# Performance work log

Hardware: AMD Instinct MI355X
Metric: run time of the kernel (lower is better)

## Reference

```python
import jax, jax.numpy as jnp
import numpy as np

IN_DIM = 256
OUT_DIM = 256
GRID_SIZE = 8
K = 3  # spline_order
LOW, UP = -1.0, 1.0
BATCH = 512


def _control_grid():
    # equally spaced control points, extended by K on each side (paper sec 2.4)
    spacing = (UP - LOW) / GRID_SIZE
    g = jnp.arange(-K, GRID_SIZE + K + 1, dtype=jnp.float32) * spacing + LOW
    # buffer shape (out_dim, in_dim, G + 2K + 1)
    return jnp.broadcast_to(g[None, None, :], (OUT_DIM, IN_DIM, g.shape[0]))


def _bspline_bases(x, grid):
    # x: (B, in_dim); grid: (out, in, T). Cox-de Boor recursion.
    xx = x[:, None, :, None]          # (B, 1, in, 1)
    g = grid[None]                    # (1, out, in, T)
    # order-0 (piecewise-constant) bases
    b = ((xx >= g[..., :-1]) & (xx < g[..., 1:])).astype(x.dtype)
    for j in range(1, K + 1):
        b = (xx - g[..., :-(j + 1)]) / (g[..., j:-1] - g[..., :-(j + 1)]) * b[..., :-1] \
          + (g[..., j + 1:] - xx) / (g[..., j + 1:] - g[..., 1:-j]) * b[..., 1:]
    return b  # (B, out, in, G + K)


def setup_inputs() -> dict:
    key = jax.random.key(0)
    k1, k2, k3 = jax.random.split(key, 3)
    x = jax.random.normal(k1, (BATCH, IN_DIM), dtype=jnp.float32)
    # xavier_normal_ on (out, in, G+K): fan_in = in*(G+K) -> std = sqrt(2/(fan_in+fan_out))
    fan_out = IN_DIM * (GRID_SIZE + K)  # torch convention: dim0 = fan_out, rest = fan_in
    fan_in = OUT_DIM * (GRID_SIZE + K)
    std = float(np.sqrt(2.0 / (fan_in + fan_out)))
    coef = jax.random.normal(k2, (OUT_DIM, IN_DIM, GRID_SIZE + K), dtype=jnp.float32) * std
    residual_weight = jax.random.normal(k3, (OUT_DIM, IN_DIM), dtype=jnp.float32) * 0.1
    univariate_weight = jnp.ones((OUT_DIM, IN_DIM), dtype=jnp.float32)
    return {"x": x, "coef": coef, "residual_weight": residual_weight,
            "univariate_weight": univariate_weight}


def reference(x, coef, residual_weight, univariate_weight):
    grid = _control_grid()
    bases = _bspline_bases(x, grid)                      # (B, out, in, G+K)
    spline = jnp.einsum('boig,oig->boi', bases, coef)    # sum over grid dim
    phi = residual_weight[None, :, :] * jax.nn.silu(x)[:, None, :] \
        + univariate_weight[None, :, :] * spline          # (B, out, in)
    return jnp.sum(phi, axis=-1)                          # (B, out)
```

## Files before the change

kernel.cpp:

```cpp
#include <hip/hip_runtime.h>
#include <hip/hip_bf16.h>

typedef unsigned short ushort_t;
typedef unsigned int uint_t;
typedef __attribute__((ext_vector_type(8))) short short8;
typedef __attribute__((ext_vector_type(4))) float f32x4;

#define IN_DIM 256
#define OUT_DIM 256
#define NSPL 11
#define KSLOT 12
#define CHUNK_I 32
#define KC (CHUNK_I * KSLOT)
#define LSTRIDE (KC + 8)
#define NCHUNK 8
#define RAWF 356

__device__ __forceinline__ uint_t pk2(float lo, float hi) {
  __hip_bfloat162 h = __float22bfloat162_rn(make_float2(lo, hi));
  union { __hip_bfloat162 h2; uint_t u; } c; c.h2 = h;
  return c.u;
}

__device__ __forceinline__ void packA_scatter(ushort_t* cb, ushort_t* dump, float xf) {
  const float t = (xf + 1.75f) * 4.0f;
  const float fJ = floorf(t);
  const int J = (int)fJ;
  const float u = t - fJ;
  const float u2 = u * u, u3 = u2 * u, um = 1.0f - u;
  const float n0 = um * um * um * (1.0f / 6.0f);
  const float n1 = 0.5f * u3 - u2 + (4.0f / 6.0f);
  const float n2 = -0.5f * u3 + 0.5f * u2 + 0.5f * u + (1.0f / 6.0f);
  const float n3 = u3 * (1.0f / 6.0f);
  const float silu = xf / (1.0f + __expf(-xf));

#pragma unroll
  for (int s = 0; s < 12; ++s) cb[s] = 0;

  const uint_t p01 = pk2(n0, n1);
  const uint_t p23 = pk2(n2, n3);
  const uint_t psl = pk2(silu, silu);

  const int base = J - 3;
  ushort_t* w0 = ((unsigned)(base + 0) <= 10u) ? (cb + base + 0) : (dump + 0);
  ushort_t* w1 = ((unsigned)(base + 1) <= 10u) ? (cb + base + 1) : (dump + 1);
  ushort_t* w2 = ((unsigned)(base + 2) <= 10u) ? (cb + base + 2) : (dump + 2);
  ushort_t* w3 = ((unsigned)(base + 3) <= 10u) ? (cb + base + 3) : (dump + 3);
  *w0 = (ushort_t)p01;
  *w1 = (ushort_t)(p01 >> 16);
  *w2 = (ushort_t)p23;
  *w3 = (ushort_t)(p23 >> 16);
  cb[11] = (ushort_t)psl;
}

__device__ __forceinline__ void packW_f32(const float* c, float us, float r, uint_t o6[6]) {
  o6[0] = pk2(us * c[0], us * c[1]);
  o6[1] = pk2(us * c[2], us * c[3]);
  o6[2] = pk2(us * c[4], us * c[5]);
  o6[3] = pk2(us * c[6], us * c[7]);
  o6[4] = pk2(us * c[8], us * c[9]);
  o6[5] = pk2(us * c[10], r);
}

__device__ __forceinline__ void writeT(ushort_t* dst, const uint_t* p) {
  uint_t* d = (uint_t*)dst;
#pragma unroll
  for (int j = 0; j < 6; ++j) d[j] = p[j];
}

__global__ __launch_bounds__(256, 2) void fused(const float* __restrict__ x,
                                                const float* __restrict__ coef,
                                                const float* __restrict__ rw,
                                                const float* __restrict__ uw,
                                                float* __restrict__ out) {
  __shared__ __attribute__((aligned(16))) ushort_t As[2][16 * LSTRIDE];
  __shared__ __attribute__((aligned(16))) ushort_t Ws[2][16 * LSTRIDE];
  __shared__ __attribute__((aligned(16))) float rawc[16][RAWF];

  const int tid = threadIdx.x;
  const int lane = tid & 63;
  const int w = tid >> 6;
  const int B = blockIdx.x;
  const int mt = B >> 4;
  const int nt = ((B & 7) << 1) | ((B >> 3) & 1);
  const int b0 = mt * 16, o0 = nt * 16;
  const int mn = lane & 15;
  const int klane = (lane >> 4) * 8;

  const int row = tid >> 4;
  const int i0 = tid & 15;

  float2 cf[11];
  float xa0, xa1, us0, us1, rr0, rr1;

#define LOADC(C)                                                              \
  {                                                                           \
    const int ib = (C) * CHUNK_I;                                             \
    xa0 = x[(b0 + row) * IN_DIM + ib + i0];                                   \
    xa1 = x[(b0 + row) * IN_DIM + ib + i0 + 16];                              \
    const int orow = o0 + row;                                                \
    us0 = uw[orow * IN_DIM + ib + i0];                                        \
    us1 = uw[orow * IN_DIM + ib + i0 + 16];                                   \
    rr0 = rw[orow * IN_DIM + ib + i0];                                        \
    rr1 = rw[orow * IN_DIM + ib + i0 + 16];                                   \
    const float2* csrc = (const float2*)(coef + ((size_t)orow * IN_DIM + ib) * NSPL); \
    _Pragma("unroll")                                                         \
    for (int j = 0; j < 11; ++j) cf[j] = csrc[i0 + j * 16];   \
  }

#define CVTSTORE                                                              \
  {                                                                           \
    float2* rrow = (float2*)&rawc[row][0];                                    \
    _Pragma("unroll")                                                         \
    for (int j = 0; j < 11; ++j) rrow[i0 + j * 16] = cf[j];                   \
  }

#define PACK(BUF)                                                             \
  {                                                                           \
    ushort_t* arow = &As[BUF][row * LSTRIDE];                                 \
    packA_scatter(arow + i0 * KSLOT, arow + KC, xa0);                         \
    packA_scatter(arow + (i0 + 16) * KSLOT, arow + KC, xa1);                  \
    uint_t p6[6];                                                             \
    packW_f32(&rawc[row][NSPL * i0], us0, rr0, p6);                           \
    writeT(&Ws[BUF][row * LSTRIDE + i0 * KSLOT], p6);                         \
    packW_f32(&rawc[row][NSPL * (i0 + 16)], us1, rr1, p6);                    \
    writeT(&Ws[BUF][row * LSTRIDE + (i0 + 16) * KSLOT], p6);                  \
  }

  f32x4 acc = {0.f, 0.f, 0.f, 0.f};

  LOADC(0)
  CVTSTORE
  PACK(0)
  __syncthreads();

  for (int c = 0; c < NCHUNK; ++c) {
    const int cur = c & 1;

    if (c + 1 < NCHUNK) { LOADC(c + 1) }
    __builtin_amdgcn_sched_barrier(0);

    __builtin_amdgcn_s_setprio(1);
#pragma unroll
    for (int s = 0; s < 3; ++s) {
      const int k = w * 96 + s * 32 + klane;
      short8 af  = *(const short8*)&As[cur][mn * LSTRIDE + k];
      short8 bfr = *(const short8*)&Ws[cur][mn * LSTRIDE + k];
      acc = __builtin_amdgcn_mfma_f32_16x16x32_bf16(af, bfr, acc, 0, 0, 0);
    }
    __builtin_amdgcn_s_setprio(0);

    if (c + 1 < NCHUNK) {
      CVTSTORE
      PACK(cur ^ 1)
    }
    __syncthreads();
  }

  f32x4* red = (f32x4*)&rawc[0][0];
  if (w > 0) red[(w - 1) * 64 + lane] = acc;
  __syncthreads();

  if (w == 0) {
    const f32x4 q0 = red[lane];
    const f32x4 q1 = red[64 + lane];
    const f32x4 q2 = red[128 + lane];
#pragma unroll
    for (int q = 0; q < 4; ++q) acc[q] += q0[q] + q1[q] + q2[q];

    const int col = o0 + mn;
    const int rbase = b0 + (lane >> 4) * 4;
#pragma unroll
    for (int r = 0; r < 4; ++r) {
      out[(size_t)(rbase + r) * OUT_DIM + col] = acc[r];
    }
  }
}

extern "C" void kernel_launch(void* const* d_in, const int* in_sizes, int n_in,
                              void* d_out, int out_size, void* d_ws, size_t ws_size,
                              hipStream_t stream) {
  const float* x    = (const float*)d_in[0];
  const float* coef = (const float*)d_in[1];
  const float* rw   = (const float*)d_in[2];
  const float* uw   = (const float*)d_in[3];
  float* out = (float*)d_out;

  fused<<<512, 256, 0, stream>>>(x, coef, rw, uw, out);
}
```

Measured before the change: 19.28 us.

## Split the input dimension across two blocks with atomic accumulation

Each output tile is now computed by two blocks, each covering half of the input dimension in 16-wide chunks. Partial results are combined with relaxed atomic adds into an output that is zeroed by a memset beforehand. The grid doubles to 1024 blocks and launch bounds rise to allow more resident blocks, which aims to raise occupancy and latency hiding. Within a chunk only two of the four waves now issue MFMAs, alternating by chunk. The cost is an extra memset launch, atomic traffic, and half-sized per-chunk work with the same number of barriers.

```diff
diff --git a/kernel.cpp b/kernel.cpp
--- a/kernel.cpp
+++ b/kernel.cpp
@@ -10,11 +10,11 @@
 #define OUT_DIM 256
 #define NSPL 11
 #define KSLOT 12
-#define CHUNK_I 32
+#define CHUNK_I 16
 #define KC (CHUNK_I * KSLOT)
 #define LSTRIDE (KC + 8)
 #define NCHUNK 8
-#define RAWF 356
+#define RAWF 180
 
 __device__ __forceinline__ uint_t pk2(float lo, float hi) {
   __hip_bfloat162 h = __float22bfloat162_rn(make_float2(lo, hi));
@@ -35,7 +35,7 @@
   const float silu = xf / (1.0f + __expf(-xf));
 
 #pragma unroll
-  for (int s = 0; s < 12; ++s) cb[s] = 0;
+  for (int z = 0; z < 12; ++z) cb[z] = 0;
 
   const uint_t p01 = pk2(n0, n1);
   const uint_t p23 = pk2(n2, n3);
@@ -68,7 +68,7 @@
   for (int j = 0; j < 6; ++j) d[j] = p[j];
 }
 
-__global__ __launch_bounds__(256, 2) void fused(const float* __restrict__ x,
+__global__ __launch_bounds__(256, 4) void fused(const float* __restrict__ x,
                                                 const float* __restrict__ coef,
                                                 const float* __restrict__ rw,
                                                 const float* __restrict__ uw,
@@ -81,50 +81,46 @@
   const int lane = tid & 63;
   const int w = tid >> 6;
   const int B = blockIdx.x;
-  const int mt = B >> 4;
-  const int nt = ((B & 7) << 1) | ((B >> 3) & 1);
+  const int T = B >> 1;
+  const int s = B & 1;
+  const int mt = T >> 4;
+  const int nt = ((T & 7) << 1) | ((T >> 3) & 1);
   const int b0 = mt * 16, o0 = nt * 16;
+  const int kb0 = s * 128;
   const int mn = lane & 15;
   const int klane = (lane >> 4) * 8;
 
   const int row = tid >> 4;
   const int i0 = tid & 15;
 
-  float2 cf[11];
-  float xa0, xa1, us0, us1, rr0, rr1;
+  float cfs[11];
+  float xa, us, rr;
 
 #define LOADC(C)                                                              \
   {                                                                           \
-    const int ib = (C) * CHUNK_I;                                             \
-    xa0 = x[(b0 + row) * IN_DIM + ib + i0];                                   \
-    xa1 = x[(b0 + row) * IN_DIM + ib + i0 + 16];                              \
+    const int ib = kb0 + (C) * CHUNK_I;                                       \
+    xa = x[(b0 + row) * IN_DIM + ib + i0];                                    \
     const int orow = o0 + row;                                                \
-    us0 = uw[orow * IN_DIM + ib + i0];                                        \
-    us1 = uw[orow * IN_DIM + ib + i0 + 16];                                   \
-    rr0 = rw[orow * IN_DIM + ib + i0];                                        \
-    rr1 = rw[orow * IN_DIM + ib + i0 + 16];                                   \
-    const float2* csrc = (const float2*)(coef + ((size_t)orow * IN_DIM + ib) * NSPL); \
+    us = uw[orow * IN_DIM + ib + i0];                                         \
+    rr = rw[orow * IN_DIM + ib + i0];                                         \
+    const float* csrc = coef + ((size_t)orow * IN_DIM + ib) * NSPL;           \
     _Pragma("unroll")                                                         \
-    for (int j = 0; j < 11; ++j) cf[j] = csrc[i0 + j * 16];   \
+    for (int j = 0; j < 11; ++j) cfs[j] = csrc[i0 + j * 16];   \
   }
 
 #define CVTSTORE                                                              \
   {                                                                           \
-    float2* rrow = (float2*)&rawc[row][0];                                    \
     _Pragma("unroll")                                                         \
-    for (int j = 0; j < 11; ++j) rrow[i0 + j * 16] = cf[j];                   \
+    for (int j = 0; j < 11; ++j) rawc[row][i0 + j * 16] = cfs[j];             \
   }
 
 #define PACK(BUF)                                                             \
   {                                                                           \
     ushort_t* arow = &As[BUF][row * LSTRIDE];                                 \
-    packA_scatter(arow + i0 * KSLOT, arow + KC, xa0);                         \
-    packA_scatter(arow + (i0 + 16) * KSLOT, arow + KC, xa1);                  \
+    packA_scatter(arow + i0 * KSLOT, arow + KC, xa);                          \
     uint_t p6[6];                                                             \
-    packW_f32(&rawc[row][NSPL * i0], us0, rr0, p6);                           \
+    packW_f32(&rawc[row][NSPL * i0], us, rr, p6);                             \
     writeT(&Ws[BUF][row * LSTRIDE + i0 * KSLOT], p6);                         \
-    packW_f32(&rawc[row][NSPL * (i0 + 16)], us1, rr1, p6);                    \
-    writeT(&Ws[BUF][row * LSTRIDE + (i0 + 16) * KSLOT], p6);                  \
   }
 
   f32x4 acc = {0.f, 0.f, 0.f, 0.f};
@@ -140,15 +136,18 @@
     if (c + 1 < NCHUNK) { LOADC(c + 1) }
     __builtin_amdgcn_sched_barrier(0);
 
-    __builtin_amdgcn_s_setprio(1);
+    if ((w >> 1) == (c & 1)) {
+      __builtin_amdgcn_s_setprio(1);
+      const int kb = (w & 1) * 96;
 #pragma unroll
-    for (int s = 0; s < 3; ++s) {
-      const int k = w * 96 + s * 32 + klane;
-      short8 af  = *(const short8*)&As[cur][mn * LSTRIDE + k];
-      short8 bfr = *(const short8*)&Ws[cur][mn * LSTRIDE + k];
-      acc = __builtin_amdgcn_mfma_f32_16x16x32_bf16(af, bfr, acc, 0, 0, 0);
+      for (int q = 0; q < 3; ++q) {
+        const int k = kb + q * 32 + klane;
+        short8 af  = *(const short8*)&As[cur][mn * LSTRIDE + k];
+        short8 bfr = *(const short8*)&Ws[cur][mn * LSTRIDE + k];
+        acc = __builtin_amdgcn_mfma_f32_16x16x32_bf16(af, bfr, acc, 0, 0, 0);
+      }
+      __builtin_amdgcn_s_setprio(0);
     }
-    __builtin_amdgcn_s_setprio(0);
 
     if (c + 1 < NCHUNK) {
       CVTSTORE
@@ -172,7 +171,8 @@
     const int rbase = b0 + (lane >> 4) * 4;
 #pragma unroll
     for (int r = 0; r < 4; ++r) {
-      out[(size_t)(rbase + r) * OUT_DIM + col] = acc[r];
+      __hip_atomic_fetch_add(&out[(size_t)(rbase + r) * OUT_DIM + col], acc[r],
+                             __ATOMIC_RELAXED, __HIP_MEMORY_SCOPE_AGENT);
     }
   }
 }
@@ -186,5 +186,6 @@
   const float* uw   = (const float*)d_in[3];
   float* out = (float*)d_out;
 
-  fused<<<512, 256, 0, stream>>>(x, coef, rw, uw, out);
+  hipMemsetAsync(out, 0, (size_t)out_size * sizeof(float), stream);
+  fused<<<1024, 256, 0, stream>>>(x, coef, rw, uw, out);
 }
```

Result: slower. 22.90 us (+18.8%).

## Prefetch global loads two chunks ahead using dual register sets

Applied to the files above, without the earlier changes.

Global loads for each input chunk now go into two alternating register sets (A and B), and the main loop is unrolled by two, so loads are issued two chunks ahead of their use instead of one. The separate convert-store and pack steps are merged into a single macro. The sched_barrier and setprio hints around the MFMAs are dropped. The aim is to hide global memory latency better, at the cost of roughly doubling the prefetch registers, which may reduce occupancy under launch_bounds(256,2).

```diff
diff --git a/kernel.cpp b/kernel.cpp
--- a/kernel.cpp
+++ b/kernel.cpp
@@ -35,7 +35,7 @@
   const float silu = xf / (1.0f + __expf(-xf));
 
 #pragma unroll
-  for (int s = 0; s < 12; ++s) cb[s] = 0;
+  for (int z = 0; z < 12; ++z) cb[z] = 0;
 
   const uint_t p01 = pk2(n0, n1);
   const uint_t p23 = pk2(n2, n3);
@@ -90,69 +90,69 @@
   const int row = tid >> 4;
   const int i0 = tid & 15;
 
-  float2 cf[11];
-  float xa0, xa1, us0, us1, rr0, rr1;
+  float2 cfA[11], cfB[11];
+  float xaA0, xaA1, usA0, usA1, rrA0, rrA1;
+  float xaB0, xaB1, usB0, usB1, rrB0, rrB1;
 
-#define LOADC(C)                                                              \
+#define LOADC(S, C)                                                           \
   {                                                                           \
     const int ib = (C) * CHUNK_I;                                             \
-    xa0 = x[(b0 + row) * IN_DIM + ib + i0];                                   \
-    xa1 = x[(b0 + row) * IN_DIM + ib + i0 + 16];                              \
+    xa##S##0 = x[(b0 + row) * IN_DIM + ib + i0];                              \
+    xa##S##1 = x[(b0 + row) * IN_DIM + ib + i0 + 16];                         \
     const int orow = o0 + row;                                                \
-    us0 = uw[orow * IN_DIM + ib + i0];                                        \
-    us1 = uw[orow * IN_DIM + ib + i0 + 16];                                   \
-    rr0 = rw[orow * IN_DIM + ib + i0];                                        \
-    rr1 = rw[orow * IN_DIM + ib + i0 + 16];                                   \
+    us##S##0 = uw[orow * IN_DIM + ib + i0];                                   \
+    us##S##1 = uw[orow * IN_DIM + ib + i0 + 16];                              \
+    rr##S##0 = rw[orow * IN_DIM + ib + i0];                                   \
+    rr##S##1 = rw[orow * IN_DIM + ib + i0 + 16];                              \
     const float2* csrc = (const float2*)(coef + ((size_t)orow * IN_DIM + ib) * NSPL); \
     _Pragma("unroll")                                                         \
-    for (int j = 0; j < 11; ++j) cf[j] = csrc[i0 + j * 16];   \
+    for (int j = 0; j < 11; ++j) cf##S[j] = csrc[i0 + j * 16];   \
   }
 
-#define CVTSTORE                                                              \
+#define CVTPACK(S, BUF)                                                       \
   {                                                                           \
     float2* rrow = (float2*)&rawc[row][0];                                    \
     _Pragma("unroll")                                                         \
-    for (int j = 0; j < 11; ++j) rrow[i0 + j * 16] = cf[j];                   \
+    for (int j = 0; j < 11; ++j) rrow[i0 + j * 16] = cf##S[j];                \
+    ushort_t* arow = &As[BUF][row * LSTRIDE];                                 \
+    packA_scatter(arow + i0 * KSLOT, arow + KC, xa##S##0);                    \
+    packA_scatter(arow + (i0 + 16) * KSLOT, arow + KC, xa##S##1);             \
+    uint_t p6[6];                                                             \
+    packW_f32(&rawc[row][NSPL * i0], us##S##0, rr##S##0, p6);                 \
+    writeT(&Ws[BUF][row * LSTRIDE + i0 * KSLOT], p6);                         \
+    packW_f32(&rawc[row][NSPL * (i0 + 16)], us##S##1, rr##S##1, p6);          \
+    writeT(&Ws[BUF][row * LSTRIDE + (i0 + 16) * KSLOT], p6);                  \
   }
 
-#define PACK(BUF)                                                             \
+#define MFMA3(BUF)                                                            \
   {                                                                           \
-    ushort_t* arow = &As[BUF][row * LSTRIDE];                                 \
-    packA_scatter(arow + i0 * KSLOT, arow + KC, xa0);                         \
-    packA_scatter(arow + (i0 + 16) * KSLOT, arow + KC, xa1);                  \
-    uint_t p6[6];                                                             \
-    packW_f32(&rawc[row][NSPL * i0], us0, rr0, p6);                           \
-    writeT(&Ws[BUF][row * LSTRIDE + i0 * KSLOT], p6);                         \
-    packW_f32(&rawc[row][NSPL * (i0 + 16)], us1, rr1, p6);                    \
-    writeT(&Ws[BUF][row * LSTRIDE + (i0 + 16) * KSLOT], p6);                  \
+    _Pragma("unroll")                                                         \
+    for (int q = 0; q < 3; ++q) {                                             \
+      const int k = w * 96 + q * 32 + klane;                                  \
+      short8 af  = *(const short8*)&As[BUF][mn * LSTRIDE + k];                \
+      short8 bfr = *(const short8*)&Ws[BUF][mn * LSTRIDE + k];                \
+      acc = __builtin_amdgcn_mfma_f32_16x16x32_bf16(af, bfr, acc, 0, 0, 0);   \
+    }                                                                         \
   }
 
   f32x4 acc = {0.f, 0.f, 0.f, 0.f};
 
-  LOADC(0)
-  CVTSTORE
-  PACK(0)
+  LOADC(A, 0)
+  CVTPACK(A, 0)
+  LOADC(B, 1)
   __syncthreads();
 
-  for (int c = 0; c < NCHUNK; ++c) {
-    const int cur = c & 1;
+#pragma unroll
+  for (int cc = 0; cc < 4; ++cc) {
+    MFMA3(0)
+    if (cc < 3) { LOADC(A, 2 * cc + 2) }
+    CVTPACK(B, 1)
+    __syncthreads();
 
-    if (c + 1 < NCHUNK) { LOADC(c + 1) }
-    __builtin_amdgcn_sched_barrier(0);
-
-    __builtin_amdgcn_s_setprio(1);
-#pragma unroll
-    for (int s = 0; s < 3; ++s) {
-      const int k = w * 96 + s * 32 + klane;
-      short8 af  = *(const short8*)&As[cur][mn * LSTRIDE + k];
-      short8 bfr = *(const short8*)&Ws[cur][mn * LSTRIDE + k];
-      acc = __builtin_amdgcn_mfma_f32_16x16x32_bf16(af, bfr, acc, 0, 0, 0);
-    }
-    __builtin_amdgcn_s_setprio(0);
-
-    if (c + 1 < NCHUNK) {
-      CVTSTORE
-      PACK(cur ^ 1)
+    MFMA3(1)
+    if (cc < 3) {
+      LOADC(B, 2 * cc + 3)
+      CVTPACK(A, 0)
     }
     __syncthreads();
   }
```

New measurement: 18.67 us. 3.2% less time.
